# Kernel optimization log

Measured on AMD Instinct MI355X. Metric: run time of the kernel, lower is better.

The kernel has to match this reference:

```python
import jax, jax.numpy as jnp
import numpy as np
import math

D = 512
LAMBDA_DRIFT = 0.3

def _sinusoid(pos, d):
    # pos: [B, T] float positions (1..T); returns [B, T, d]
    half = d // 2
    div = jnp.exp(-math.log(10000.0) * (2.0 * jnp.arange(half, dtype=jnp.float32) / d))
    ang = pos[..., None] * div  # [B,T,half]
    pe = jnp.stack([jnp.sin(ang), jnp.cos(ang)], axis=-1)  # [B,T,half,2]
    return pe.reshape(pos.shape + (d,))

def _lin(x, W, b):
    return x @ W + b

def setup_inputs() -> dict:
    key = jax.random.key(0)
    ks = jax.random.split(key, 30)
    B, T, L = 4, 16, 1024
    def w(k, fan_in, fan_out):
        return jax.random.normal(k, (fan_in, fan_out), dtype=jnp.float32) / np.sqrt(fan_in)
    inp = {
        'x': jax.random.normal(ks[0], (B, L, D), dtype=jnp.float32),
        'memory_snapshot': jax.random.normal(ks[1], (B, T, L, D), dtype=jnp.float32),
        'delta_W': w(ks[2], D, D), 'delta_b': jnp.zeros((D,), jnp.float32),
        'xproj_W': w(ks[3], D, D), 'xproj_b': jnp.zeros((D,), jnp.float32),
        'phys_W': w(ks[4], D, D), 'phys_b': jnp.zeros((D,), jnp.float32),
        'gate_W': w(ks[5], 3 * D, D), 'gate_b': jnp.zeros((D,), jnp.float32),
        'outp_W': w(ks[6], D, D), 'outp_b': jnp.zeros((D,), jnp.float32),
        'seq_W': w(ks[7], D, D), 'seq_b': jnp.zeros((D,), jnp.float32),
        'q_W': w(ks[8], D, D), 'q_b': jnp.zeros((D,), jnp.float32),
        'mem_W': w(ks[9], D, D), 'mem_b': jnp.zeros((D,), jnp.float32),
        'curd_W': w(ks[10], D, D), 'curd_b': jnp.zeros((D,), jnp.float32),
        'memd_W': w(ks[11], D, D), 'memd_b': jnp.zeros((D,), jnp.float32),
        'fuse_W': w(ks[12], 2 * D, D), 'fuse_b': jnp.zeros((D,), jnp.float32),
    }
    return inp

def reference(x, memory_snapshot,
              delta_W, delta_b, xproj_W, xproj_b, phys_W, phys_b,
              gate_W, gate_b, outp_W, outp_b, seq_W, seq_b,
              q_W, q_b, mem_W, mem_b, curd_W, curd_b,
              memd_W, memd_b, fuse_W, fuse_b):
    B, T, L, Dm = memory_snapshot.shape
    # physical trajectory = last memory slot
    x_phys = memory_snapshot[:, -1]                      # [B,L,D]
    # --- DriftCorrectionExtractor ---
    delta = x - x_phys
    delta_feat = _lin(delta, delta_W, delta_b)
    x_feat = _lin(x, xproj_W, xproj_b)
    phys_feat = _lin(x_phys, phys_W, phys_b)
    g = jax.nn.sigmoid(_lin(jnp.concatenate([delta, x, x_phys], -1), gate_W, gate_b))
    raw_memory = _lin(g * delta_feat + (1.0 - g) * (x_feat - phys_feat), outp_W, outp_b)
    # --- sequential positional embedding on memory time axis ---
    pos = jnp.broadcast_to(jnp.arange(1, T + 1, dtype=jnp.float32)[None, :], (B, T))
    pos_emb = _lin(_sinusoid(pos, Dm), seq_W, seq_b)     # [B,T,D]
    memory = memory_snapshot + pos_emb[:, :, None, :]    # [B,T,L,D]
    # --- content score ---
    q_global = _lin((x + raw_memory).mean(axis=1), q_W, q_b)        # [B,D]
    memory_global = _lin(memory.mean(axis=2), mem_W, mem_b)          # [B,T,D]
    content_score = jnp.einsum('bd,btd->bt', q_global, memory_global) / math.sqrt(Dm)
    # --- drift score ---
    cur_drift = _lin(delta.mean(axis=1), curd_W, curd_b)             # [B,D]
    mem_delta = jnp.concatenate(
        [memory[:, :1], memory[:, 1:] - memory[:, :-1]], axis=1)     # [B,T,L,D]
    mem_drift = _lin(mem_delta.mean(axis=2), memd_W, memd_b)         # [B,T,D]
    drift_score = -jnp.mean((cur_drift[:, None, :] - mem_drift) ** 2, axis=-1)
    time_attn = jax.nn.softmax(content_score + LAMBDA_DRIFT * drift_score, axis=1)
    enhanced = jnp.einsum('bt,btld->bld', time_attn, memory)
    fuse_g = jax.nn.sigmoid(_lin(jnp.concatenate([x, enhanced], -1), fuse_W, fuse_b))
    return x + raw_memory + fuse_g * enhanced
```

## Files before the change

kernel.cpp:

```cpp
#include <hip/hip_runtime.h>
#include <hip/hip_bf16.h>
#include <math.h>

typedef __attribute__((ext_vector_type(8))) short short8;
typedef __attribute__((ext_vector_type(4))) float floatx4;

__device__ __forceinline__ short f2bits(float f) {
    union { float f; unsigned u; } cv; cv.f = f;
    unsigned u = cv.u;
    u += 0x7fffu + ((u >> 16) & 1u);
    return (short)(u >> 16);
}

__device__ __forceinline__ floatx4 mfma16(short8 a, short8 b, floatx4 c) {
    return __builtin_amdgcn_mfma_f32_16x16x32_bf16(a, b, c, 0, 0, 0);
}

typedef const __attribute__((address_space(1))) unsigned int* gas_ptr;
typedef __attribute__((address_space(3))) unsigned int* las_ptr;

__device__ __forceinline__ void gl2lds16(const short* g, short* l) {
    __builtin_amdgcn_global_load_lds((gas_ptr)g, (las_ptr)l, 16, 0, 0);
}

__global__ __launch_bounds__(256) void k_tr(
    const float* __restrict__ w_delta, const float* __restrict__ w_xproj,
    const float* __restrict__ w_phys,  const float* __restrict__ w_outp,
    const float* __restrict__ w_gate,  const float* __restrict__ w_fuse,
    short* __restrict__ bt_delta, short* __restrict__ bt_xproj,
    short* __restrict__ bt_phys,  short* __restrict__ bt_outp,
    short* __restrict__ bt_gate,  short* __restrict__ bt_fuse)
{
    int gid = blockIdx.x * 256 + threadIdx.x;
    const float* src; short* dst; int K; int i;
    if (gid < 262144)       { src = w_delta; dst = bt_delta; K = 512;  i = gid; }
    else if (gid < 524288)  { src = w_xproj; dst = bt_xproj; K = 512;  i = gid - 262144; }
    else if (gid < 786432)  { src = w_phys;  dst = bt_phys;  K = 512;  i = gid - 524288; }
    else if (gid < 1048576) { src = w_outp;  dst = bt_outp;  K = 512;  i = gid - 786432; }
    else if (gid < 1835008) { src = w_gate;  dst = bt_gate;  K = 1536; i = gid - 1048576; }
    else                    { src = w_fuse;  dst = bt_fuse;  K = 1024; i = gid - 1835008; }
    int k = i >> 9, n = i & 511;
    dst[(size_t)n * K + k] = f2bits(src[i]);
}

__global__ __launch_bounds__(256) void k_prep(const float* __restrict__ x,
                                              const float* __restrict__ ms,
                                              short* __restrict__ A1)
{
    int gid = blockIdx.x * 256 + threadIdx.x;
    int r = gid >> 7;
    int c4 = (gid & 127) << 2;
    int b = r >> 10, l = r & 1023;
    float4 xv = *(const float4*)(x + (size_t)r * 512 + c4);
    float4 pv = *(const float4*)(ms + ((size_t)(b * 16 + 15) * 1024 + l) * 512 + c4);
    short4 xb, pb, db;
    xb.x = f2bits(xv.x); xb.y = f2bits(xv.y); xb.z = f2bits(xv.z); xb.w = f2bits(xv.w);
    pb.x = f2bits(pv.x); pb.y = f2bits(pv.y); pb.z = f2bits(pv.z); pb.w = f2bits(pv.w);
    db.x = f2bits(xv.x - pv.x); db.y = f2bits(xv.y - pv.y);
    db.z = f2bits(xv.z - pv.z); db.w = f2bits(xv.w - pv.w);
    short* row = A1 + (size_t)r * 1536;
    *(short4*)(row + c4) = db;
    *(short4*)(row + 512 + c4) = xb;
    *(short4*)(row + 1024 + c4) = pb;
}

__global__ __launch_bounds__(128) void k_msum(const float* __restrict__ ms, float* __restrict__ msum)
{
    int bt = blockIdx.x >> 3;
    int chunk = blockIdx.x & 7;
    int c4 = threadIdx.x << 2;
    const float* base = ms + ((size_t)bt * 1024 + chunk * 128) * 512 + c4;
    float a0 = 0, a1 = 0, a2 = 0, a3 = 0;
    for (int l = 0; l < 128; ++l) {
        float4 v = *(const float4*)(base + (size_t)l * 512);
        a0 += v.x; a1 += v.y; a2 += v.z; a3 += v.w;
    }
    float* dst = msum + bt * 512 + c4;
    atomicAdd(dst + 0, a0); atomicAdd(dst + 1, a1);
    atomicAdd(dst + 2, a2); atomicAdd(dst + 3, a3);
}

__global__ __launch_bounds__(128) void k_dmean(const float* __restrict__ x, const float* __restrict__ ms,
                                               float* __restrict__ dmean)
{
    int b = blockIdx.x >> 3, chunk = blockIdx.x & 7;
    int c4 = threadIdx.x << 2;
    float a0 = 0, a1 = 0, a2 = 0, a3 = 0;
    for (int l = 0; l < 128; ++l) {
        int r = b * 1024 + chunk * 128 + l;
        int lr = chunk * 128 + l;
        float4 xv = *(const float4*)(x + (size_t)r * 512 + c4);
        float4 pv = *(const float4*)(ms + ((size_t)(b * 16 + 15) * 1024 + lr) * 512 + c4);
        a0 += xv.x - pv.x; a1 += xv.y - pv.y; a2 += xv.z - pv.z; a3 += xv.w - pv.w;
    }
    float* dst = dmean + b * 512 + c4;
    atomicAdd(dst + 0, a0); atomicAdd(dst + 1, a1);
    atomicAdd(dst + 2, a2); atomicAdd(dst + 3, a3);
}

__global__ __launch_bounds__(128) void k_rmean(const float* __restrict__ x, const float* __restrict__ rawm,
                                               float* __restrict__ xrm)
{
    int b = blockIdx.x >> 3, chunk = blockIdx.x & 7;
    int c4 = threadIdx.x << 2;
    float a0 = 0, a1 = 0, a2 = 0, a3 = 0;
    for (int l = 0; l < 128; ++l) {
        size_t idx = ((size_t)(b * 1024 + chunk * 128 + l)) * 512 + c4;
        float4 v = *(const float4*)(x + idx);
        float4 rm = *(const float4*)(rawm + idx);
        a0 += v.x + rm.x; a1 += v.y + rm.y; a2 += v.z + rm.z; a3 += v.w + rm.w;
    }
    float* dst = xrm + b * 512 + c4;
    atomicAdd(dst + 0, a0); atomicAdd(dst + 1, a1);
    atomicAdd(dst + 2, a2); atomicAdd(dst + 3, a3);
}

__global__ __launch_bounds__(256) void gemm_h_t(
    const short* __restrict__ A1,
    const short* __restrict__ BTd, const short* __restrict__ BTx,
    const short* __restrict__ BTp, const short* __restrict__ BTg,
    const float* __restrict__ bd, const float* __restrict__ bx,
    const float* __restrict__ bp, const float* __restrict__ bg,
    short* __restrict__ H)
{
    __shared__ __align__(16) short As[2048], Bgs[2048], Bss[2048];
    int bm = blockIdx.x >> 3, bn = blockIdx.x & 7;
    int t = threadIdx.x;
    int lane = t & 63;
    int wm = (t >> 6) & 1, wn = t >> 7;
    int l15 = lane & 15, quad = lane >> 4;

    int srow = t >> 2;
    int sc = ((t & 3) - (srow >> 1)) & 3;
    const short* ga  = A1  + (size_t)(bm * 64 + srow) * 1536 + sc * 8;
    const short* ggb = BTg + (size_t)(bn * 64 + srow) * 1536 + sc * 8;
    const short* gsd = BTd + (size_t)(bn * 64 + srow) * 512 + sc * 8;
    const short* gsx = BTx + (size_t)(bn * 64 + srow) * 512 + sc * 8;
    const short* gsp = BTp + (size_t)(bn * 64 + srow) * 512 + sc * 8;
    short* la  = As  + t * 8;
    short* lgb = Bgs + t * 8;
    short* lsb = Bss + t * 8;

    int arow = wm * 32 + l15;
    int brow = wn * 32 + l15;
    const short* ra0 = As  + arow * 32 + ((quad + (arow >> 1)) & 3) * 8;
    const short* ra1 = ra0 + 512;
    const short* rg0 = Bgs + brow * 32 + ((quad + (brow >> 1)) & 3) * 8;
    const short* rg1 = rg0 + 512;
    const short* rs0 = Bss + brow * 32 + ((quad + (brow >> 1)) & 3) * 8;
    const short* rs1 = rs0 + 512;

    floatx4 g00 = {0,0,0,0}, g01 = {0,0,0,0}, g10 = {0,0,0,0}, g11 = {0,0,0,0};
    floatx4 d00 = {0,0,0,0}, d01 = {0,0,0,0}, d10 = {0,0,0,0}, d11 = {0,0,0,0};
    floatx4 x00 = {0,0,0,0}, x01 = {0,0,0,0}, x10 = {0,0,0,0}, x11 = {0,0,0,0};
    floatx4 p00 = {0,0,0,0}, p01 = {0,0,0,0}, p10 = {0,0,0,0}, p11 = {0,0,0,0};

#define HPHASE(GSB, S00, S01, S10, S11, KBASE)                                  \
    for (int k0 = 0; k0 < 512; k0 += 32) {                                      \
        gl2lds16(ga + KBASE + k0, la);                                          \
        gl2lds16(ggb + KBASE + k0, lgb);                                        \
        gl2lds16(GSB + k0, lsb);                                                \
        __syncthreads();                                                        \
        short8 a0 = *(const short8*)ra0; short8 a1 = *(const short8*)ra1;       \
        short8 c0 = *(const short8*)rg0; short8 c1 = *(const short8*)rg1;       \
        short8 e0 = *(const short8*)rs0; short8 e1 = *(const short8*)rs1;       \
        g00 = mfma16(a0, c0, g00); g01 = mfma16(a0, c1, g01);                   \
        g10 = mfma16(a1, c0, g10); g11 = mfma16(a1, c1, g11);                   \
        S00 = mfma16(a0, e0, S00); S01 = mfma16(a0, e1, S01);                   \
        S10 = mfma16(a1, e0, S10); S11 = mfma16(a1, e1, S11);                   \
        __syncthreads();                                                        \
    }

    HPHASE(gsd, d00, d01, d10, d11, 0)
    HPHASE(gsx, x00, x01, x10, x11, 512)
    HPHASE(gsp, p00, p01, p10, p11, 1024)
#undef HPHASE

    floatx4 G[2][2] = {{g00, g01}, {g10, g11}};
    floatx4 Dd[2][2] = {{d00, d01}, {d10, d11}};
    floatx4 Xx[2][2] = {{x00, x01}, {x10, x11}};
    floatx4 Pp[2][2] = {{p00, p01}, {p10, p11}};
    int colb = bn * 64 + wn * 32 + l15;
    int rowb = bm * 64 + wm * 32 + quad * 4;
    for (int ni = 0; ni < 2; ++ni) {
        int col = colb + ni * 16;
        float vbd = bd[col], vbx = bx[col], vbp = bp[col], vbg = bg[col];
        for (int mi = 0; mi < 2; ++mi) {
            for (int r = 0; r < 4; ++r) {
                int row = rowb + mi * 16 + r;
                float gv = 1.f / (1.f + expf(-(G[mi][ni][r] + vbg)));
                float h = gv * (Dd[mi][ni][r] + vbd)
                        + (1.f - gv) * ((Xx[mi][ni][r] + vbx) - (Pp[mi][ni][r] + vbp));
                H[(size_t)row * 512 + col] = f2bits(h);
            }
        }
    }
}

template<int MODE>
__global__ __launch_bounds__(256) void gemm_t(
    const short* __restrict__ A, int lda,
    const short* __restrict__ BT, int K,
    const float* __restrict__ bias, float* __restrict__ C,
    const float* __restrict__ xsrc, const float* __restrict__ rawm,
    const float* __restrict__ enh, float* __restrict__ outp)
{
    __shared__ __align__(16) short As[2048], Bs[2048];
    int bm = blockIdx.x >> 3, bn = blockIdx.x & 7;
    int t = threadIdx.x;
    int lane = t & 63;
    int wm = (t >> 6) & 1, wn = t >> 7;
    int l15 = lane & 15, quad = lane >> 4;

    int srow = t >> 2;
    int sc = ((t & 3) - (srow >> 1)) & 3;
    const short* ga = A + (size_t)(bm * 64 + srow) * lda + sc * 8;
    const short* gb = BT + (size_t)(bn * 64 + srow) * K + sc * 8;
    short* la = As + t * 8;
    short* lb = Bs + t * 8;

    int arow = wm * 32 + l15;
    int brow = wn * 32 + l15;
    const short* ra0 = As + arow * 32 + ((quad + (arow >> 1)) & 3) * 8;
    const short* ra1 = ra0 + 512;
    const short* rb0 = Bs + brow * 32 + ((quad + (brow >> 1)) & 3) * 8;
    const short* rb1 = rb0 + 512;

    floatx4 a00 = {0,0,0,0}, a01 = {0,0,0,0}, a10 = {0,0,0,0}, a11 = {0,0,0,0};

    for (int k0 = 0; k0 < K; k0 += 32) {
        gl2lds16(ga + k0, la);
        gl2lds16(gb + k0, lb);
        __syncthreads();
        short8 a0 = *(const short8*)ra0; short8 a1 = *(const short8*)ra1;
        short8 b0 = *(const short8*)rb0; short8 b1 = *(const short8*)rb1;
        a00 = mfma16(a0, b0, a00); a01 = mfma16(a0, b1, a01);
        a10 = mfma16(a1, b0, a10); a11 = mfma16(a1, b1, a11);
        __syncthreads();
    }

    floatx4 Acc[2][2] = {{a00, a01}, {a10, a11}};
    int colb = bn * 64 + wn * 32 + l15;
    int rowb = bm * 64 + wm * 32 + quad * 4;
    for (int ni = 0; ni < 2; ++ni) {
        int col = colb + ni * 16;
        float bv = bias[col];
        for (int mi = 0; mi < 2; ++mi) {
            for (int r = 0; r < 4; ++r) {
                int row = rowb + mi * 16 + r;
                size_t idx = (size_t)row * 512 + col;
                float v = Acc[mi][ni][r] + bv;
                if (MODE == 0) {
                    C[idx] = v;
                } else {
                    float fg = 1.f / (1.f + expf(-v));
                    outp[idx] = xsrc[idx] + rawm[idx] + fg * enh[idx];
                }
            }
        }
    }
}

__global__ __launch_bounds__(256) void k_pe(const float* __restrict__ seqW, const float* __restrict__ seqb,
                                            float* __restrict__ pe_proj)
{
    __shared__ float pe[512];
    int t = blockIdx.x;
    for (int d = threadIdx.x; d < 512; d += 256) {
        int i = d >> 1;
        float div = expf(-9.210340371976184f * (2.f * i / 512.f));
        float ang = (float)(t + 1) * div;
        pe[d] = (d & 1) ? cosf(ang) : sinf(ang);
    }
    __syncthreads();
    for (int n = threadIdx.x; n < 512; n += 256) {
        float acc = 0.f;
        for (int d = 0; d < 512; ++d) acc += pe[d] * seqW[(size_t)d * 512 + n];
        pe_proj[t * 512 + n] = acc + seqb[n];
    }
}

__global__ __launch_bounds__(256) void k_mid(const float* __restrict__ msum, const float* __restrict__ pe_proj,
                                             const float* __restrict__ memW, const float* __restrict__ memb,
                                             const float* __restrict__ memdW, const float* __restrict__ memdb,
                                             const float* __restrict__ xrm, const float* __restrict__ qW,
                                             const float* __restrict__ qb,
                                             const float* __restrict__ dmean, const float* __restrict__ curdW,
                                             const float* __restrict__ curdb,
                                             float* __restrict__ mg, float* __restrict__ mdrift,
                                             float* __restrict__ qg, float* __restrict__ curd)
{
    __shared__ float s0[512], s1[512];
    int bi = blockIdx.x;
    const float invL = 1.f / 1024.f;
    if (bi < 64) {
        int t = bi & 15;
        for (int d = threadIdx.x; d < 512; d += 256) {
            float mm = msum[bi * 512 + d] * invL + pe_proj[t * 512 + d];
            float prev = (t > 0) ? (msum[(bi - 1) * 512 + d] * invL + pe_proj[(t - 1) * 512 + d]) : 0.f;
            s0[d] = mm; s1[d] = mm - prev;
        }
        __syncthreads();
        for (int n = threadIdx.x; n < 512; n += 256) {
            float a0 = 0.f, a1 = 0.f;
            for (int d = 0; d < 512; ++d) {
                a0 += s0[d] * memW[(size_t)d * 512 + n];
                a1 += s1[d] * memdW[(size_t)d * 512 + n];
            }
            mg[bi * 512 + n] = a0 + memb[n];
            mdrift[bi * 512 + n] = a1 + memdb[n];
        }
    } else if (bi < 68) {
        int b = bi - 64;
        for (int d = threadIdx.x; d < 512; d += 256) s0[d] = xrm[b * 512 + d] * invL;
        __syncthreads();
        for (int n = threadIdx.x; n < 512; n += 256) {
            float a = 0.f;
            for (int d = 0; d < 512; ++d) a += s0[d] * qW[(size_t)d * 512 + n];
            qg[b * 512 + n] = a + qb[n];
        }
    } else {
        int b = bi - 68;
        for (int d = threadIdx.x; d < 512; d += 256) s0[d] = dmean[b * 512 + d] * invL;
        __syncthreads();
        for (int n = threadIdx.x; n < 512; n += 256) {
            float a = 0.f;
            for (int d = 0; d < 512; ++d) a += s0[d] * curdW[(size_t)d * 512 + n];
            curd[b * 512 + n] = a + curdb[n];
        }
    }
}

__global__ __launch_bounds__(256) void k_attn(const float* __restrict__ qg, const float* __restrict__ mg,
                                              const float* __restrict__ curd, const float* __restrict__ mdrift,
                                              const float* __restrict__ pe_proj,
                                              float* __restrict__ attn, float* __restrict__ pe_att)
{
    int b = blockIdx.x;
    __shared__ float sq[512], sc[512], sscore[16], sattn[16];
    for (int d = threadIdx.x; d < 512; d += 256) { sq[d] = qg[b * 512 + d]; sc[d] = curd[b * 512 + d]; }
    __syncthreads();
    int wv = threadIdx.x >> 6, lane = threadIdx.x & 63;
    for (int t = wv; t < 16; t += 4) {
        float cs = 0.f, dsum = 0.f;
        const float* mgp = mg + (size_t)(b * 16 + t) * 512;
        const float* mdp = mdrift + (size_t)(b * 16 + t) * 512;
        for (int d = lane; d < 512; d += 64) {
            cs += sq[d] * mgp[d];
            float df_ = sc[d] - mdp[d];
            dsum += df_ * df_;
        }
        for (int off = 32; off; off >>= 1) { cs += __shfl_down(cs, off); dsum += __shfl_down(dsum, off); }
        if (lane == 0) sscore[t] = cs * (1.f / 22.627416997969522f) + 0.3f * (-dsum / 512.f);
    }
    __syncthreads();
    if (threadIdx.x == 0) {
        float mx = -1e30f;
        for (int t = 0; t < 16; ++t) mx = fmaxf(mx, sscore[t]);
        float s = 0.f;
        for (int t = 0; t < 16; ++t) { float e = expf(sscore[t] - mx); sattn[t] = e; s += e; }
        for (int t = 0; t < 16; ++t) { sattn[t] /= s; attn[b * 16 + t] = sattn[t]; }
    }
    __syncthreads();
    for (int n = threadIdx.x; n < 512; n += 256) {
        float a = 0.f;
        for (int t = 0; t < 16; ++t) a += sattn[t] * pe_proj[t * 512 + n];
        pe_att[b * 512 + n] = a;
    }
}

__global__ __launch_bounds__(128) void k_enh(const float* __restrict__ ms, const float* __restrict__ x,
                                             const float* __restrict__ attn, const float* __restrict__ pe_att,
                                             float* __restrict__ enh, short* __restrict__ A2)
{
    int r = blockIdx.x;
    int b = r >> 10, l = r & 1023;
    __shared__ float sa[16];
    if (threadIdx.x < 16) sa[threadIdx.x] = attn[b * 16 + threadIdx.x];
    __syncthreads();
    int c4 = threadIdx.x << 2;
    float4 pa = *(const float4*)(pe_att + b * 512 + c4);
    float a0 = pa.x, a1 = pa.y, a2 = pa.z, a3 = pa.w;
    const float* base = ms + ((size_t)(b * 16) * 1024 + l) * 512 + c4;
    for (int t = 0; t < 16; ++t) {
        float4 v = *(const float4*)(base + (size_t)t * 1024 * 512);
        float w = sa[t];
        a0 += w * v.x; a1 += w * v.y; a2 += w * v.z; a3 += w * v.w;
    }
    size_t oi = (size_t)r * 512 + c4;
    float4 ef; ef.x = a0; ef.y = a1; ef.z = a2; ef.w = a3;
    *(float4*)(enh + oi) = ef;
    float4 xv = *(const float4*)(x + oi);
    short4 xb, eb;
    xb.x = f2bits(xv.x); xb.y = f2bits(xv.y); xb.z = f2bits(xv.z); xb.w = f2bits(xv.w);
    eb.x = f2bits(a0); eb.y = f2bits(a1); eb.z = f2bits(a2); eb.w = f2bits(a3);
    short* arow = A2 + (size_t)r * 1024;
    *(short4*)(arow + c4) = xb;
    *(short4*)(arow + 512 + c4) = eb;
}

extern "C" void kernel_launch(void* const* d_in, const int* in_sizes, int n_in,
                              void* d_out, int out_size, void* d_ws, size_t ws_size,
                              hipStream_t stream)
{
    const float* x       = (const float*)d_in[0];
    const float* ms      = (const float*)d_in[1];
    const float* delta_W = (const float*)d_in[2];  const float* delta_b = (const float*)d_in[3];
    const float* xproj_W = (const float*)d_in[4];  const float* xproj_b = (const float*)d_in[5];
    const float* phys_W  = (const float*)d_in[6];  const float* phys_b  = (const float*)d_in[7];
    const float* gate_W  = (const float*)d_in[8];  const float* gate_b  = (const float*)d_in[9];
    const float* outp_W  = (const float*)d_in[10]; const float* outp_b  = (const float*)d_in[11];
    const float* seq_W   = (const float*)d_in[12]; const float* seq_b   = (const float*)d_in[13];
    const float* q_W     = (const float*)d_in[14]; const float* q_b     = (const float*)d_in[15];
    const float* mem_W   = (const float*)d_in[16]; const float* mem_b   = (const float*)d_in[17];
    const float* curd_W  = (const float*)d_in[18]; const float* curd_b  = (const float*)d_in[19];
    const float* memd_W  = (const float*)d_in[20]; const float* memd_b  = (const float*)d_in[21];
    const float* fuse_W  = (const float*)d_in[22]; const float* fuse_b  = (const float*)d_in[23];
    float* out = (float*)d_out;
    char* wsb = (char*)d_ws;

    short* BT_delta = (short*)(wsb + 0);
    short* BT_xproj = (short*)(wsb + 524288);
    short* BT_phys  = (short*)(wsb + 1048576);
    short* BT_outp  = (short*)(wsb + 1572864);
    short* BT_gate  = (short*)(wsb + 2097152);
    short* BT_fuse  = (short*)(wsb + 3670016);
    short* A1       = (short*)(wsb + 4718592);
    short* H        = (short*)(wsb + 17301504);
    float* RAWM     = (float*)(wsb + 21495808);
    float* ENH      = (float*)(wsb + 29884416);
    short* A2       = (short*)(wsb + 38273024);
    float* MSUM     = (float*)(wsb + 46661632);
    float* DMEAN    = (float*)(wsb + 46792704);
    float* XRM      = (float*)(wsb + 46800896);
    float* PEPROJ   = (float*)(wsb + 46809088);
    float* MG       = (float*)(wsb + 46841856);
    float* MDRIFT   = (float*)(wsb + 46972928);
    float* QG       = (float*)(wsb + 47104000);
    float* CURD     = (float*)(wsb + 47112192);
    float* ATTN     = (float*)(wsb + 47120384);
    float* PEATT    = (float*)(wsb + 47121408);

    hipMemsetAsync(wsb + 46661632, 0, 131072 + 8192 + 8192, stream);

    k_tr<<<9216, 256, 0, stream>>>(delta_W, xproj_W, phys_W, outp_W, gate_W, fuse_W,
                                   BT_delta, BT_xproj, BT_phys, BT_outp, BT_gate, BT_fuse);
    k_pe<<<16, 256, 0, stream>>>(seq_W, seq_b, PEPROJ);
    k_prep<<<2048, 256, 0, stream>>>(x, ms, A1);
    k_msum<<<512, 128, 0, stream>>>(ms, MSUM);
    k_dmean<<<32, 128, 0, stream>>>(x, ms, DMEAN);

    gemm_h_t<<<512, 256, 0, stream>>>(A1, BT_delta, BT_xproj, BT_phys, BT_gate,
                                      delta_b, xproj_b, phys_b, gate_b, H);
    gemm_t<0><<<512, 256, 0, stream>>>(H, 512, BT_outp, 512, outp_b, RAWM,
                                       nullptr, nullptr, nullptr, nullptr);
    k_rmean<<<32, 128, 0, stream>>>(x, RAWM, XRM);

    k_mid<<<72, 256, 0, stream>>>(MSUM, PEPROJ, mem_W, mem_b, memd_W, memd_b,
                                  XRM, q_W, q_b, DMEAN, curd_W, curd_b,
                                  MG, MDRIFT, QG, CURD);
    k_attn<<<4, 256, 0, stream>>>(QG, MG, CURD, MDRIFT, PEPROJ, ATTN, PEATT);
    k_enh<<<4096, 128, 0, stream>>>(ms, x, ATTN, PEATT, ENH, A2);

    gemm_t<2><<<512, 256, 0, stream>>>(A2, 1024, BT_fuse, 1024, fuse_b, nullptr,
                                       x, RAWM, ENH, out);
}
```

Measured before the change: 496.3 us.

## Tile weight transpose through LDS and batch small matvecs over four rows

Replaces the element-wise weight transpose with a 32x32 LDS-tiled transpose, so global reads are float4 and writes are short4 and coalesced instead of strided scalar stores. It also splits the small mid-stage projections into a row-building kernel and a matvec kernel. Each block of the new kernel computes four input rows against one float4-loaded weight stream, with the K dimension split across two half-blocks and summed through LDS. This cuts redundant weight reads, since each weight matrix was previously reread by 16 blocks. The cost is one extra kernel launch and a staging buffer.

```diff
diff --git a/kernel.cpp b/kernel.cpp
--- a/kernel.cpp
+++ b/kernel.cpp
@@ -23,7 +23,7 @@
     __builtin_amdgcn_global_load_lds((gas_ptr)g, (las_ptr)l, 16, 0, 0);
 }
 
-__global__ __launch_bounds__(256) void k_tr(
+__global__ __launch_bounds__(256) void k_tr2(
     const float* __restrict__ w_delta, const float* __restrict__ w_xproj,
     const float* __restrict__ w_phys,  const float* __restrict__ w_outp,
     const float* __restrict__ w_gate,  const float* __restrict__ w_fuse,
@@ -31,16 +31,29 @@
     short* __restrict__ bt_phys,  short* __restrict__ bt_outp,
     short* __restrict__ bt_gate,  short* __restrict__ bt_fuse)
 {
-    int gid = blockIdx.x * 256 + threadIdx.x;
-    const float* src; short* dst; int K; int i;
-    if (gid < 262144)       { src = w_delta; dst = bt_delta; K = 512;  i = gid; }
-    else if (gid < 524288)  { src = w_xproj; dst = bt_xproj; K = 512;  i = gid - 262144; }
-    else if (gid < 786432)  { src = w_phys;  dst = bt_phys;  K = 512;  i = gid - 524288; }
-    else if (gid < 1048576) { src = w_outp;  dst = bt_outp;  K = 512;  i = gid - 786432; }
-    else if (gid < 1835008) { src = w_gate;  dst = bt_gate;  K = 1536; i = gid - 1048576; }
-    else                    { src = w_fuse;  dst = bt_fuse;  K = 1024; i = gid - 1835008; }
-    int k = i >> 9, n = i & 511;
-    dst[(size_t)n * K + k] = f2bits(src[i]);
+    __shared__ float sf[32 * 33];
+    int id = blockIdx.x;
+    const float* W; short* BT; int K; int local;
+    if (id < 256)        { W = w_delta; BT = bt_delta; K = 512;  local = id; }
+    else if (id < 512)   { W = w_xproj; BT = bt_xproj; K = 512;  local = id - 256; }
+    else if (id < 768)   { W = w_phys;  BT = bt_phys;  K = 512;  local = id - 512; }
+    else if (id < 1024)  { W = w_outp;  BT = bt_outp;  K = 512;  local = id - 768; }
+    else if (id < 1792)  { W = w_gate;  BT = bt_gate;  K = 1536; local = id - 1024; }
+    else                 { W = w_fuse;  BT = bt_fuse;  K = 1024; local = id - 1792; }
+    int kt = local >> 4, nt = local & 15;
+    int t = threadIdx.x;
+    int r = t >> 3, c = (t & 7) * 4;
+    float4 v = *(const float4*)(W + (size_t)(kt * 32 + r) * 512 + nt * 32 + c);
+    sf[r * 33 + c + 0] = v.x; sf[r * 33 + c + 1] = v.y;
+    sf[r * 33 + c + 2] = v.z; sf[r * 33 + c + 3] = v.w;
+    __syncthreads();
+    int n = t >> 3, k4 = (t & 7) * 4;
+    short4 o;
+    o.x = f2bits(sf[(k4 + 0) * 33 + n]);
+    o.y = f2bits(sf[(k4 + 1) * 33 + n]);
+    o.z = f2bits(sf[(k4 + 2) * 33 + n]);
+    o.w = f2bits(sf[(k4 + 3) * 33 + n]);
+    *(short4*)(BT + (size_t)(nt * 32 + n) * K + kt * 32 + k4) = o;
 }
 
 __global__ __launch_bounds__(256) void k_prep(const float* __restrict__ x,
@@ -280,54 +293,99 @@
     }
 }
 
-__global__ __launch_bounds__(256) void k_mid(const float* __restrict__ msum, const float* __restrict__ pe_proj,
-                                             const float* __restrict__ memW, const float* __restrict__ memb,
-                                             const float* __restrict__ memdW, const float* __restrict__ memdb,
-                                             const float* __restrict__ xrm, const float* __restrict__ qW,
-                                             const float* __restrict__ qb,
-                                             const float* __restrict__ dmean, const float* __restrict__ curdW,
-                                             const float* __restrict__ curdb,
-                                             float* __restrict__ mg, float* __restrict__ mdrift,
-                                             float* __restrict__ qg, float* __restrict__ curd)
-{
-    __shared__ float s0[512], s1[512];
-    int bi = blockIdx.x;
+__global__ __launch_bounds__(128) void k_sbuild(const float* __restrict__ msum,
+                                                const float* __restrict__ pe_proj,
+                                                const float* __restrict__ xrm,
+                                                const float* __restrict__ dmean,
+                                                float* __restrict__ SM)
+{
+    int row = blockIdx.x;
+    int c4 = threadIdx.x << 2;
     const float invL = 1.f / 1024.f;
-    if (bi < 64) {
-        int t = bi & 15;
-        for (int d = threadIdx.x; d < 512; d += 256) {
-            float mm = msum[bi * 512 + d] * invL + pe_proj[t * 512 + d];
-            float prev = (t > 0) ? (msum[(bi - 1) * 512 + d] * invL + pe_proj[(t - 1) * 512 + d]) : 0.f;
-            s0[d] = mm; s1[d] = mm - prev;
+    float4 o;
+    if (row < 64) {
+        int tt = row & 15;
+        float4 m = *(const float4*)(msum + row * 512 + c4);
+        float4 p = *(const float4*)(pe_proj + tt * 512 + c4);
+        o.x = m.x * invL + p.x; o.y = m.y * invL + p.y;
+        o.z = m.z * invL + p.z; o.w = m.w * invL + p.w;
+    } else if (row < 128) {
+        int j = row - 64, tt = j & 15;
+        float4 m = *(const float4*)(msum + j * 512 + c4);
+        float4 p = *(const float4*)(pe_proj + tt * 512 + c4);
+        o.x = m.x * invL + p.x; o.y = m.y * invL + p.y;
+        o.z = m.z * invL + p.z; o.w = m.w * invL + p.w;
+        if (tt > 0) {
+            float4 m2 = *(const float4*)(msum + (j - 1) * 512 + c4);
+            float4 p2 = *(const float4*)(pe_proj + (tt - 1) * 512 + c4);
+            o.x -= m2.x * invL + p2.x; o.y -= m2.y * invL + p2.y;
+            o.z -= m2.z * invL + p2.z; o.w -= m2.w * invL + p2.w;
         }
-        __syncthreads();
-        for (int n = threadIdx.x; n < 512; n += 256) {
-            float a0 = 0.f, a1 = 0.f;
-            for (int d = 0; d < 512; ++d) {
-                a0 += s0[d] * memW[(size_t)d * 512 + n];
-                a1 += s1[d] * memdW[(size_t)d * 512 + n];
-            }
-            mg[bi * 512 + n] = a0 + memb[n];
-            mdrift[bi * 512 + n] = a1 + memdb[n];
-        }
-    } else if (bi < 68) {
-        int b = bi - 64;
-        for (int d = threadIdx.x; d < 512; d += 256) s0[d] = xrm[b * 512 + d] * invL;
-        __syncthreads();
-        for (int n = threadIdx.x; n < 512; n += 256) {
-            float a = 0.f;
-            for (int d = 0; d < 512; ++d) a += s0[d] * qW[(size_t)d * 512 + n];
-            qg[b * 512 + n] = a + qb[n];
-        }
+    } else if (row < 132) {
+        float4 m = *(const float4*)(xrm + (row - 128) * 512 + c4);
+        o.x = m.x * invL; o.y = m.y * invL; o.z = m.z * invL; o.w = m.w * invL;
     } else {
-        int b = bi - 68;
-        for (int d = threadIdx.x; d < 512; d += 256) s0[d] = dmean[b * 512 + d] * invL;
-        __syncthreads();
-        for (int n = threadIdx.x; n < 512; n += 256) {
-            float a = 0.f;
-            for (int d = 0; d < 512; ++d) a += s0[d] * curdW[(size_t)d * 512 + n];
-            curd[b * 512 + n] = a + curdb[n];
-        }
+        float4 m = *(const float4*)(dmean + (row - 132) * 512 + c4);
+        o.x = m.x * invL; o.y = m.y * invL; o.z = m.z * invL; o.w = m.w * invL;
+    }
+    *(float4*)(SM + row * 512 + c4) = o;
+}
+
+__global__ __launch_bounds__(256) void k_mid2(const float* __restrict__ SM,
+                                              const float* __restrict__ memW,  const float* __restrict__ memb,
+                                              const float* __restrict__ memdW, const float* __restrict__ memdb,
+                                              const float* __restrict__ qW,    const float* __restrict__ qb,
+                                              const float* __restrict__ curdW, const float* __restrict__ curdb,
+                                              float* __restrict__ mg, float* __restrict__ mdrift,
+                                              float* __restrict__ qg, float* __restrict__ curd)
+{
+    __shared__ float sS[4 * 512];
+    __shared__ float part[128 * 16];
+    int blk = blockIdx.x;
+    const float* W; const float* bias; const float* S; float* out;
+    if (blk < 16)      { W = memW;  bias = memb;  S = SM + blk * 4 * 512;          out = mg + blk * 4 * 512; }
+    else if (blk < 32) { W = memdW; bias = memdb; S = SM + (64 + (blk - 16) * 4) * 512; out = mdrift + (blk - 16) * 4 * 512; }
+    else if (blk == 32){ W = qW;    bias = qb;    S = SM + 128 * 512;              out = qg; }
+    else               { W = curdW; bias = curdb; S = SM + 132 * 512;              out = curd; }
+    int t = threadIdx.x;
+    for (int i = t * 4; i < 2048; i += 1024) *(float4*)(sS + i) = *(const float4*)(S + i);
+    __syncthreads();
+    int tn = t & 127, dph = t >> 7;
+    int n4 = tn * 4;
+    float4 acc0 = {0,0,0,0}, acc1 = {0,0,0,0}, acc2 = {0,0,0,0}, acc3 = {0,0,0,0};
+    const float* wp = W + (size_t)(dph * 256) * 512 + n4;
+    const float* sp = sS + dph * 256;
+#pragma unroll 4
+    for (int d = 0; d < 256; ++d) {
+        float4 w = *(const float4*)(wp + (size_t)d * 512);
+        float s0 = sp[d], s1 = sp[512 + d], s2 = sp[1024 + d], s3 = sp[1536 + d];
+        acc0.x += s0 * w.x; acc0.y += s0 * w.y; acc0.z += s0 * w.z; acc0.w += s0 * w.w;
+        acc1.x += s1 * w.x; acc1.y += s1 * w.y; acc1.z += s1 * w.z; acc1.w += s1 * w.w;
+        acc2.x += s2 * w.x; acc2.y += s2 * w.y; acc2.z += s2 * w.z; acc2.w += s2 * w.w;
+        acc3.x += s3 * w.x; acc3.y += s3 * w.y; acc3.z += s3 * w.z; acc3.w += s3 * w.w;
+    }
+    if (dph == 1) {
+        *(float4*)(part + tn * 16 + 0)  = acc0;
+        *(float4*)(part + tn * 16 + 4)  = acc1;
+        *(float4*)(part + tn * 16 + 8)  = acc2;
+        *(float4*)(part + tn * 16 + 12) = acc3;
+    }
+    __syncthreads();
+    if (dph == 0) {
+        float4 bv = *(const float4*)(bias + n4);
+        float4 p0 = *(const float4*)(part + tn * 16 + 0);
+        float4 p1 = *(const float4*)(part + tn * 16 + 4);
+        float4 p2 = *(const float4*)(part + tn * 16 + 8);
+        float4 p3 = *(const float4*)(part + tn * 16 + 12);
+        float4 o0, o1, o2, o3;
+        o0.x = acc0.x + p0.x + bv.x; o0.y = acc0.y + p0.y + bv.y; o0.z = acc0.z + p0.z + bv.z; o0.w = acc0.w + p0.w + bv.w;
+        o1.x = acc1.x + p1.x + bv.x; o1.y = acc1.y + p1.y + bv.y; o1.z = acc1.z + p1.z + bv.z; o1.w = acc1.w + p1.w + bv.w;
+        o2.x = acc2.x + p2.x + bv.x; o2.y = acc2.y + p2.y + bv.y; o2.z = acc2.z + p2.z + bv.z; o2.w = acc2.w + p2.w + bv.w;
+        o3.x = acc3.x + p3.x + bv.x; o3.y = acc3.y + p3.y + bv.y; o3.z = acc3.z + p3.z + bv.z; o3.w = acc3.w + p3.w + bv.w;
+        *(float4*)(out + 0 * 512 + n4) = o0;
+        *(float4*)(out + 1 * 512 + n4) = o1;
+        *(float4*)(out + 2 * 512 + n4) = o2;
+        *(float4*)(out + 3 * 512 + n4) = o3;
     }
 }
 
@@ -440,11 +498,12 @@
     float* CURD     = (float*)(wsb + 47112192);
     float* ATTN     = (float*)(wsb + 47120384);
     float* PEATT    = (float*)(wsb + 47121408);
+    float* SM       = (float*)(wsb + 47129600);
 
     hipMemsetAsync(wsb + 46661632, 0, 131072 + 8192 + 8192, stream);
 
-    k_tr<<<9216, 256, 0, stream>>>(delta_W, xproj_W, phys_W, outp_W, gate_W, fuse_W,
-                                   BT_delta, BT_xproj, BT_phys, BT_outp, BT_gate, BT_fuse);
+    k_tr2<<<2304, 256, 0, stream>>>(delta_W, xproj_W, phys_W, outp_W, gate_W, fuse_W,
+                                    BT_delta, BT_xproj, BT_phys, BT_outp, BT_gate, BT_fuse);
     k_pe<<<16, 256, 0, stream>>>(seq_W, seq_b, PEPROJ);
     k_prep<<<2048, 256, 0, stream>>>(x, ms, A1);
     k_msum<<<512, 128, 0, stream>>>(ms, MSUM);
@@ -456,9 +515,10 @@
                                        nullptr, nullptr, nullptr, nullptr);
     k_rmean<<<32, 128, 0, stream>>>(x, RAWM, XRM);
 
-    k_mid<<<72, 256, 0, stream>>>(MSUM, PEPROJ, mem_W, mem_b, memd_W, memd_b,
-                                  XRM, q_W, q_b, DMEAN, curd_W, curd_b,
-                                  MG, MDRIFT, QG, CURD);
+    k_sbuild<<<136, 128, 0, stream>>>(MSUM, PEPROJ, XRM, DMEAN, SM);
+    k_mid2<<<34, 256, 0, stream>>>(SM, mem_W, mem_b, memd_W, memd_b,
+                                   q_W, q_b, curd_W, curd_b,
+                                   MG, MDRIFT, QG, CURD);
     k_attn<<<4, 256, 0, stream>>>(QG, MG, CURD, MDRIFT, PEPROJ, ATTN, PEATT);
     k_enh<<<4096, 128, 0, stream>>>(ms, x, ATTN, PEATT, ENH, A2);
 
```

Result: faster. 448.5 us (-9.6%).
